# Optimization experiments

Measured on AMD Instinct MI355X. Metric: run time of the kernel, lower is better.

Reference implementation:

```python
import jax, jax.numpy as jnp
import numpy as np

B, N, P, L = 8, 512, 32, 3  # batch, n_node, hidden p, n_layer
NODE_FEAT = 3               # 2 + extra_feat_size(=1)
W_STD = 0.01


def setup_inputs() -> dict:
    key = jax.random.key(0)
    ks = jax.random.split(key, 8)
    x = jax.random.uniform(ks[0], (B, N), dtype=jnp.float32)
    adjacency = jax.random.uniform(ks[1], (B, N, N), dtype=jnp.float32)
    weights = jax.random.normal(ks[2], (B, N, N), dtype=jnp.float32)
    extra_feat = jax.random.normal(ks[3], (B, N, 1), dtype=jnp.float32)
    # per-layer parameters, stacked on a leading layer axis
    t1 = jax.random.normal(ks[4], (L, P, NODE_FEAT), dtype=jnp.float32) * W_STD
    t2 = jax.random.normal(ks[5], (L, P, P), dtype=jnp.float32) * W_STD
    t3 = jax.random.normal(ks[6], (L, P, P), dtype=jnp.float32) * W_STD
    t4 = jax.random.normal(ks[7], (L, P, 4), dtype=jnp.float32) * W_STD
    return {"x": x, "adjacency": adjacency, "weights": weights,
            "extra_feat": extra_feat, "t1": t1, "t2": t2, "t3": t3, "t4": t4}


def reference(x, adjacency, weights, extra_feat, t1, t2, t3, t4):
    b, n = x.shape
    # node features: [1-x, ones, extra_feat]  -> (B, 3, N)
    node_feat = jnp.stack([1.0 - x, jnp.ones_like(x), extra_feat[..., 0]], axis=1)
    # edge features are built from .data in torch => detached
    xd = jax.lax.stop_gradient(x)
    wd = jax.lax.stop_gradient(weights)
    s = 2.0 * xd - 1.0
    is_edge_cut = -(s[:, :, None] * s[:, None, :] - 1.0) * 0.5  # (B,N,N)
    edge_feat = jnp.stack([
        jnp.broadcast_to(xd[:, :, None], (b, n, n)),  # channel 0: x expanded
        wd,                                           # channel 1: weights
        is_edge_cut,                                  # channel 2
        jnp.ones((b, n, n), dtype=x.dtype),           # channel 3: ones
    ], axis=1)  # (B, 4, N, N)

    mu = jnp.zeros((b, t1.shape[1], n), dtype=x.dtype)  # (B, P, N)
    for i in range(t1.shape[0]):
        term1 = jnp.einsum('pf,bfn->bpn', t1[i], node_feat)
        term2 = jnp.einsum('bpn,bnm->bpm',
                           jnp.einsum('pq,bqn->bpn', t2[i], mu), adjacency)
        # skinny 4->P matmul over N*N edges, relu, sum over last axis
        t31 = jax.nn.relu(jnp.einsum('pe,benm->bpnm', t4[i], edge_feat)).sum(-1)  # (B,P,N)
        term3 = jnp.einsum('pq,bqn->bpn', t3[i], t31)
        mu = jax.nn.relu(term1 + term2 + term3)
    return mu
```

## Files before the change

### kernel.cpp

```cpp
#include <hip/hip_runtime.h>

#define BB 8
#define NN 512
#define PP 32
#define SLOT (BB*NN*PP)

__global__ __launch_bounds__(256) void k_phaseA(
    const float* __restrict__ x, const float* __restrict__ wts,
    const float* __restrict__ extra, const float* __restrict__ t1,
    const float* __restrict__ t2, const float* __restrict__ t3,
    const float* __restrict__ t4, float* __restrict__ ws)
{
    const int tid  = threadIdx.x;
    const int wv   = tid >> 6;
    const int lane = tid & 63;
    const int blk  = blockIdx.x;
    const int l  = blk >> 10;
    const int b  = (blk >> 7) & 7;
    const int nt = blk & 127;
    const int n  = nt*4 + wv;

    __shared__ float part[4][32][68];
    __shared__ float cbuf[4][32];

    const float* xrow = x + b*NN;
    const float* wrow = wts + ((size_t)b*NN + n)*NN;
    const float4 wa = *(const float4*)(wrow + lane*4);
    const float4 wb = *(const float4*)(wrow + 256 + lane*4);
    const float4 xa = *(const float4*)(xrow + lane*4);
    const float4 xb = *(const float4*)(xrow + 256 + lane*4);
    const float4 sa = { 2.f*xa.x-1.f, 2.f*xa.y-1.f, 2.f*xa.z-1.f, 2.f*xa.w-1.f };
    const float4 sb = { 2.f*xb.x-1.f, 2.f*xb.y-1.f, 2.f*xb.z-1.f, 2.f*xb.w-1.f };
    const float xn = xrow[n];
    const float en = extra[b*NN + n];
    const float sn = 2.f*xn - 1.f;

    const float* t4l = t4 + l*(PP*4);
#pragma unroll
    for (int p = 0; p < 32; ++p) {
        const float c0 = t4l[p*4+0], Ay = t4l[p*4+1];
        const float Bz = t4l[p*4+2], c3 = t4l[p*4+3];
        const float Cc = fmaf(c0, xn, fmaf(0.5f, Bz, c3));
        const float Bc = -0.5f*Bz*sn;
        float a0, a1;
        a0  = fmaxf(0.f, fmaf(Ay, wa.x, fmaf(Bc, sa.x, Cc)));
        a1  = fmaxf(0.f, fmaf(Ay, wa.y, fmaf(Bc, sa.y, Cc)));
        a0 += fmaxf(0.f, fmaf(Ay, wa.z, fmaf(Bc, sa.z, Cc)));
        a1 += fmaxf(0.f, fmaf(Ay, wa.w, fmaf(Bc, sa.w, Cc)));
        a0 += fmaxf(0.f, fmaf(Ay, wb.x, fmaf(Bc, sb.x, Cc)));
        a1 += fmaxf(0.f, fmaf(Ay, wb.y, fmaf(Bc, sb.y, Cc)));
        a0 += fmaxf(0.f, fmaf(Ay, wb.z, fmaf(Bc, sb.z, Cc)));
        a1 += fmaxf(0.f, fmaf(Ay, wb.w, fmaf(Bc, sb.w, Cc)));
        part[wv][p][lane] = a0 + a1;
    }

    const int p2 = lane & 31, h = lane >> 5;
    float r = 0.f;
#pragma unroll
    for (int k = 0; k < 8; ++k) {
        const float4 v = *(const float4*)&part[wv][p2][h*32 + k*4];
        r += (v.x + v.y) + (v.z + v.w);
    }
    r += __shfl_xor(r, 32, 64);
    cbuf[wv][p2] = r;

    const float* t3r = t3 + l*(PP*PP) + p2*32;
    float term3 = 0.f;
#pragma unroll
    for (int q = 0; q < 8; ++q) {
        const float4 tv = *(const float4*)(t3r + q*4);
        const float4 cv = *(const float4*)&cbuf[wv][q*4];
        term3 = fmaf(tv.x,cv.x, fmaf(tv.y,cv.y, fmaf(tv.z,cv.z, fmaf(tv.w,cv.w, term3))));
    }
    const float* t1r = t1 + l*(PP*3) + p2*3;
    const float term1 = fmaf(t1r[0], 1.f-xn, fmaf(t1r[2], en, t1r[1]));
    const float basev = term1 + term3;

    if (l == 0) {
        const float mu0 = fmaxf(basev, 0.f);
        cbuf[wv][p2] = mu0;
        const float* t2r = t2 + PP*PP + p2*32;
        float s0 = 0.f;
#pragma unroll
        for (int q = 0; q < 8; ++q) {
            const float4 tv = *(const float4*)(t2r + q*4);
            const float4 cv = *(const float4*)&cbuf[wv][q*4];
            s0 = fmaf(tv.x,cv.x, fmaf(tv.y,cv.y, fmaf(tv.z,cv.z, fmaf(tv.w,cv.w, s0))));
        }
        if (h == 0) ws[2*SLOT + ((size_t)(b*NN + n))*PP + p2] = s0;
    } else {
        float* dst = ws + (l == 1 ? 0 : SLOT);
        if (h == 0) dst[((size_t)(b*NN + n))*PP + p2] = basev;
    }
}

__global__ __launch_bounds__(512) void k_layer(
    const float* __restrict__ adj, const float* __restrict__ t2l,
    const float* __restrict__ basein, const float* __restrict__ tmp2in,
    float* __restrict__ tmp2out, float* __restrict__ dout, int final_)
{
    const int tid  = threadIdx.x;
    const int b    = blockIdx.x >> 3;
    const int jt   = blockIdx.x & 7;
    const int j0   = jt * 64;
    const int w    = __builtin_amdgcn_readfirstlane(tid >> 6);
    const int lane = tid & 63;
    const int hh   = w >> 2;
    const int ww   = w & 3;

    __shared__ float part[2][32][66];
    __shared__ float mub[32][66];

    float acc[8];
#pragma unroll
    for (int i = 0; i < 8; ++i) acc[i] = 0.f;

    const float* adjp = adj + (size_t)b*NN*NN + (size_t)(hh*256)*NN + j0 + lane;
    const float* trp  = tmp2in + (size_t)b*NN*PP + (size_t)(hh*256)*PP + ww*8;

#pragma unroll 8
    for (int n = 0; n < 256; ++n) {
        const float av = adjp[(size_t)n*NN];
        const float4 ta = *(const float4*)(trp + n*PP);
        const float4 tb = *(const float4*)(trp + n*PP + 4);
        acc[0] = fmaf(ta.x, av, acc[0]);
        acc[1] = fmaf(ta.y, av, acc[1]);
        acc[2] = fmaf(ta.z, av, acc[2]);
        acc[3] = fmaf(ta.w, av, acc[3]);
        acc[4] = fmaf(tb.x, av, acc[4]);
        acc[5] = fmaf(tb.y, av, acc[5]);
        acc[6] = fmaf(tb.z, av, acc[6]);
        acc[7] = fmaf(tb.w, av, acc[7]);
    }
#pragma unroll
    for (int i = 0; i < 8; ++i) part[hh][ww*8 + i][lane] = acc[i];
    __syncthreads();

    const int j  = tid & 63;
    const int pg = tid >> 6;
    const float4 bs = *(const float4*)(basein + ((size_t)b*NN + j0 + j)*PP + pg*4);
    float r0 = part[0][pg*4+0][j] + part[1][pg*4+0][j] + bs.x;
    float r1 = part[0][pg*4+1][j] + part[1][pg*4+1][j] + bs.y;
    float r2 = part[0][pg*4+2][j] + part[1][pg*4+2][j] + bs.z;
    float r3 = part[0][pg*4+3][j] + part[1][pg*4+3][j] + bs.w;
    r0 = fmaxf(r0, 0.f); r1 = fmaxf(r1, 0.f);
    r2 = fmaxf(r2, 0.f); r3 = fmaxf(r3, 0.f);

    if (final_) {
        dout[((size_t)b*PP + pg*4+0)*NN + j0 + j] = r0;
        dout[((size_t)b*PP + pg*4+1)*NN + j0 + j] = r1;
        dout[((size_t)b*PP + pg*4+2)*NN + j0 + j] = r2;
        dout[((size_t)b*PP + pg*4+3)*NN + j0 + j] = r3;
    } else {
        mub[pg*4+0][j] = r0;
        mub[pg*4+1][j] = r1;
        mub[pg*4+2][j] = r2;
        mub[pg*4+3][j] = r3;
        __syncthreads();

        const float* t0 = t2l + (pg*4+0)*32;
        const float* t1r = t2l + (pg*4+1)*32;
        const float* t2r = t2l + (pg*4+2)*32;
        const float* t3r = t2l + (pg*4+3)*32;
        float o0 = 0.f, o1 = 0.f, o2 = 0.f, o3 = 0.f;
#pragma unroll
        for (int qc = 0; qc < 8; ++qc) {
            const float m0 = mub[qc*4+0][j];
            const float m1 = mub[qc*4+1][j];
            const float m2 = mub[qc*4+2][j];
            const float m3 = mub[qc*4+3][j];
            const float4 a0 = *(const float4*)(t0  + qc*4);
            const float4 a1 = *(const float4*)(t1r + qc*4);
            const float4 a2 = *(const float4*)(t2r + qc*4);
            const float4 a3 = *(const float4*)(t3r + qc*4);
            o0 = fmaf(a0.x,m0, fmaf(a0.y,m1, fmaf(a0.z,m2, fmaf(a0.w,m3, o0))));
            o1 = fmaf(a1.x,m0, fmaf(a1.y,m1, fmaf(a1.z,m2, fmaf(a1.w,m3, o1))));
            o2 = fmaf(a2.x,m0, fmaf(a2.y,m1, fmaf(a2.z,m2, fmaf(a2.w,m3, o2))));
            o3 = fmaf(a3.x,m0, fmaf(a3.y,m1, fmaf(a3.z,m2, fmaf(a3.w,m3, o3))));
        }
        const float4 ov = { o0, o1, o2, o3 };
        *(float4*)(tmp2out + ((size_t)b*NN + j0 + j)*PP + pg*4) = ov;
    }
}

extern "C" void kernel_launch(void* const* d_in, const int* in_sizes, int n_in,
                              void* d_out, int out_size, void* d_ws, size_t ws_size,
                              hipStream_t stream) {
    const float* x     = (const float*)d_in[0];
    const float* adj   = (const float*)d_in[1];
    const float* wts   = (const float*)d_in[2];
    const float* extra = (const float*)d_in[3];
    const float* t1    = (const float*)d_in[4];
    const float* t2    = (const float*)d_in[5];
    const float* t3    = (const float*)d_in[6];
    const float* t4    = (const float*)d_in[7];
    float* out = (float*)d_out;
    float* ws  = (float*)d_ws;

    float* slotA = ws;
    float* slotB = ws + SLOT;
    float* slotC = ws + 2*SLOT;

    hipLaunchKernelGGL(k_phaseA, dim3(3*BB*128), dim3(256), 0, stream,
                       x, wts, extra, t1, t2, t3, t4, ws);
    hipLaunchKernelGGL(k_layer, dim3(BB*8), dim3(512), 0, stream,
                       adj, t2 + 2*PP*PP, slotA, slotC, slotA, (float*)nullptr, 0);
    hipLaunchKernelGGL(k_layer, dim3(BB*8), dim3(512), 0, stream,
                       adj, t2, slotB, slotA, (float*)nullptr, out, 1);
}
```

Before: 146.2 us.

## Split adjacency matmul along N into partial kernels plus reduce; batch phaseA work

Each adjacency layer is split into a partial-product kernel with 256 blocks, each handling a quarter of the N reduction with tmp2 staged in LDS, followed by a small reduce kernel that sums the partials, adds the base, applies relu and computes the next t2 projection. The previous layout used only 64 blocks. Phase A now runs 1024 blocks that each loop over three (layer, batch, node) units and reads t4 from LDS. This raises parallelism on the adjacency pass at the cost of two extra launches and a round trip of the partial sums through global memory.

```diff
diff --git a/kernel.cpp b/kernel.cpp
--- a/kernel.cpp
+++ b/kernel.cpp
@@ -3,7 +3,12 @@
 #define BB 8
 #define NN 512
 #define PP 32
-#define SLOT (BB*NN*PP)
+
+#define OFF_BASE1 0
+#define OFF_BASE2 131072
+#define OFF_T21   262144
+#define OFF_T22   393216
+#define OFF_PART  524288
 
 __global__ __launch_bounds__(256) void k_phaseA(
     const float* __restrict__ x, const float* __restrict__ wts,
@@ -14,115 +19,126 @@
     const int tid  = threadIdx.x;
     const int wv   = tid >> 6;
     const int lane = tid & 63;
-    const int blk  = blockIdx.x;
-    const int l  = blk >> 10;
-    const int b  = (blk >> 7) & 7;
-    const int nt = blk & 127;
-    const int n  = nt*4 + wv;
-
+
+    __shared__ float4 t4lds[3][32];
     __shared__ float part[4][32][68];
     __shared__ float cbuf[4][32];
 
-    const float* xrow = x + b*NN;
-    const float* wrow = wts + ((size_t)b*NN + n)*NN;
-    const float4 wa = *(const float4*)(wrow + lane*4);
-    const float4 wb = *(const float4*)(wrow + 256 + lane*4);
-    const float4 xa = *(const float4*)(xrow + lane*4);
-    const float4 xb = *(const float4*)(xrow + 256 + lane*4);
-    const float4 sa = { 2.f*xa.x-1.f, 2.f*xa.y-1.f, 2.f*xa.z-1.f, 2.f*xa.w-1.f };
-    const float4 sb = { 2.f*xb.x-1.f, 2.f*xb.y-1.f, 2.f*xb.z-1.f, 2.f*xb.w-1.f };
-    const float xn = xrow[n];
-    const float en = extra[b*NN + n];
-    const float sn = 2.f*xn - 1.f;
-
-    const float* t4l = t4 + l*(PP*4);
-#pragma unroll
-    for (int p = 0; p < 32; ++p) {
-        const float c0 = t4l[p*4+0], Ay = t4l[p*4+1];
-        const float Bz = t4l[p*4+2], c3 = t4l[p*4+3];
-        const float Cc = fmaf(c0, xn, fmaf(0.5f, Bz, c3));
-        const float Bc = -0.5f*Bz*sn;
-        float a0, a1;
-        a0  = fmaxf(0.f, fmaf(Ay, wa.x, fmaf(Bc, sa.x, Cc)));
-        a1  = fmaxf(0.f, fmaf(Ay, wa.y, fmaf(Bc, sa.y, Cc)));
-        a0 += fmaxf(0.f, fmaf(Ay, wa.z, fmaf(Bc, sa.z, Cc)));
-        a1 += fmaxf(0.f, fmaf(Ay, wa.w, fmaf(Bc, sa.w, Cc)));
-        a0 += fmaxf(0.f, fmaf(Ay, wb.x, fmaf(Bc, sb.x, Cc)));
-        a1 += fmaxf(0.f, fmaf(Ay, wb.y, fmaf(Bc, sb.y, Cc)));
-        a0 += fmaxf(0.f, fmaf(Ay, wb.z, fmaf(Bc, sb.z, Cc)));
-        a1 += fmaxf(0.f, fmaf(Ay, wb.w, fmaf(Bc, sb.w, Cc)));
-        part[wv][p][lane] = a0 + a1;
-    }
-
-    const int p2 = lane & 31, h = lane >> 5;
-    float r = 0.f;
-#pragma unroll
-    for (int k = 0; k < 8; ++k) {
-        const float4 v = *(const float4*)&part[wv][p2][h*32 + k*4];
-        r += (v.x + v.y) + (v.z + v.w);
-    }
-    r += __shfl_xor(r, 32, 64);
-    cbuf[wv][p2] = r;
-
-    const float* t3r = t3 + l*(PP*PP) + p2*32;
-    float term3 = 0.f;
-#pragma unroll
-    for (int q = 0; q < 8; ++q) {
-        const float4 tv = *(const float4*)(t3r + q*4);
-        const float4 cv = *(const float4*)&cbuf[wv][q*4];
-        term3 = fmaf(tv.x,cv.x, fmaf(tv.y,cv.y, fmaf(tv.z,cv.z, fmaf(tv.w,cv.w, term3))));
-    }
-    const float* t1r = t1 + l*(PP*3) + p2*3;
-    const float term1 = fmaf(t1r[0], 1.f-xn, fmaf(t1r[2], en, t1r[1]));
-    const float basev = term1 + term3;
-
-    if (l == 0) {
-        const float mu0 = fmaxf(basev, 0.f);
-        cbuf[wv][p2] = mu0;
-        const float* t2r = t2 + PP*PP + p2*32;
-        float s0 = 0.f;
+    if (tid < 96) t4lds[0][tid] = ((const float4*)t4)[tid];
+    __syncthreads();
+
+    const int wgid = blockIdx.x * 4 + wv;
+#pragma unroll 1
+    for (int k = 0; k < 3; ++k) {
+        const int u = wgid * 3 + k;
+        const int l = u >> 12;
+        const int b = (u >> 9) & 7;
+        const int n = u & 511;
+
+        const float* xrow = x + b*NN;
+        const float* wrow = wts + ((size_t)b*NN + n)*NN;
+        const float4 wa = *(const float4*)(wrow + lane*4);
+        const float4 wb = *(const float4*)(wrow + 256 + lane*4);
+        const float4 xa = *(const float4*)(xrow + lane*4);
+        const float4 xb = *(const float4*)(xrow + 256 + lane*4);
+        const float4 sa = { 2.f*xa.x-1.f, 2.f*xa.y-1.f, 2.f*xa.z-1.f, 2.f*xa.w-1.f };
+        const float4 sb = { 2.f*xb.x-1.f, 2.f*xb.y-1.f, 2.f*xb.z-1.f, 2.f*xb.w-1.f };
+        const float xn = xrow[n];
+        const float en = extra[b*NN + n];
+        const float sn = 2.f*xn - 1.f;
+
+#pragma unroll
+        for (int p = 0; p < 32; ++p) {
+            const float4 c4 = t4lds[l][p];
+            const float Ay = c4.y;
+            const float Cc = fmaf(c4.x, xn, fmaf(0.5f, c4.z, c4.w));
+            const float Bc = -0.5f*c4.z*sn;
+            float a0, a1;
+            a0  = fmaxf(0.f, fmaf(Ay, wa.x, fmaf(Bc, sa.x, Cc)));
+            a1  = fmaxf(0.f, fmaf(Ay, wa.y, fmaf(Bc, sa.y, Cc)));
+            a0 += fmaxf(0.f, fmaf(Ay, wa.z, fmaf(Bc, sa.z, Cc)));
+            a1 += fmaxf(0.f, fmaf(Ay, wa.w, fmaf(Bc, sa.w, Cc)));
+            a0 += fmaxf(0.f, fmaf(Ay, wb.x, fmaf(Bc, sb.x, Cc)));
+            a1 += fmaxf(0.f, fmaf(Ay, wb.y, fmaf(Bc, sb.y, Cc)));
+            a0 += fmaxf(0.f, fmaf(Ay, wb.z, fmaf(Bc, sb.z, Cc)));
+            a1 += fmaxf(0.f, fmaf(Ay, wb.w, fmaf(Bc, sb.w, Cc)));
+            part[wv][p][lane] = a0 + a1;
+        }
+
+        const int p2 = lane & 31, h = lane >> 5;
+        float r = 0.f;
 #pragma unroll
         for (int q = 0; q < 8; ++q) {
-            const float4 tv = *(const float4*)(t2r + q*4);
+            const float4 v = *(const float4*)&part[wv][p2][h*32 + q*4];
+            r += (v.x + v.y) + (v.z + v.w);
+        }
+        r += __shfl_xor(r, 32, 64);
+        cbuf[wv][p2] = r;
+
+        const float* t3r = t3 + l*(PP*PP) + p2*32;
+        float term3 = 0.f;
+#pragma unroll
+        for (int q = 0; q < 8; ++q) {
+            const float4 tv = *(const float4*)(t3r + q*4);
             const float4 cv = *(const float4*)&cbuf[wv][q*4];
-            s0 = fmaf(tv.x,cv.x, fmaf(tv.y,cv.y, fmaf(tv.z,cv.z, fmaf(tv.w,cv.w, s0))));
-        }
-        if (h == 0) ws[2*SLOT + ((size_t)(b*NN + n))*PP + p2] = s0;
-    } else {
-        float* dst = ws + (l == 1 ? 0 : SLOT);
-        if (h == 0) dst[((size_t)(b*NN + n))*PP + p2] = basev;
-    }
-}
-
-__global__ __launch_bounds__(512) void k_layer(
-    const float* __restrict__ adj, const float* __restrict__ t2l,
-    const float* __restrict__ basein, const float* __restrict__ tmp2in,
-    float* __restrict__ tmp2out, float* __restrict__ dout, int final_)
+            term3 = fmaf(tv.x,cv.x, fmaf(tv.y,cv.y, fmaf(tv.z,cv.z, fmaf(tv.w,cv.w, term3))));
+        }
+        const float* t1r = t1 + l*(PP*3) + p2*3;
+        const float term1 = fmaf(t1r[0], 1.f-xn, fmaf(t1r[2], en, t1r[1]));
+        const float basev = term1 + term3;
+
+        if (l == 0) {
+            const float mu0 = fmaxf(basev, 0.f);
+            cbuf[wv][p2] = mu0;
+            const float* t2r = t2 + PP*PP + p2*32;
+            float s0 = 0.f;
+#pragma unroll
+            for (int q = 0; q < 8; ++q) {
+                const float4 tv = *(const float4*)(t2r + q*4);
+                const float4 cv = *(const float4*)&cbuf[wv][q*4];
+                s0 = fmaf(tv.x,cv.x, fmaf(tv.y,cv.y, fmaf(tv.z,cv.z, fmaf(tv.w,cv.w, s0))));
+            }
+            if (h == 0) ws[OFF_T21 + ((size_t)(b*NN + n))*PP + p2] = s0;
+        } else {
+            float* dst = ws + (l == 1 ? OFF_BASE1 : OFF_BASE2);
+            if (h == 0) dst[((size_t)(b*NN + n))*PP + p2] = basev;
+        }
+    }
+}
+
+__global__ __launch_bounds__(512) void k_partial(
+    const float* __restrict__ adj, const float* __restrict__ tmp2in,
+    float* __restrict__ partout, int b_, int unused)
 {
-    const int tid  = threadIdx.x;
-    const int b    = blockIdx.x >> 3;
-    const int jt   = blockIdx.x & 7;
-    const int j0   = jt * 64;
-    const int w    = __builtin_amdgcn_readfirstlane(tid >> 6);
-    const int lane = tid & 63;
-    const int hh   = w >> 2;
-    const int ww   = w & 3;
-
-    __shared__ float part[2][32][66];
-    __shared__ float mub[32][66];
-
-    float acc[8];
-#pragma unroll
-    for (int i = 0; i < 8; ++i) acc[i] = 0.f;
-
-    const float* adjp = adj + (size_t)b*NN*NN + (size_t)(hh*256)*NN + j0 + lane;
-    const float* trp  = tmp2in + (size_t)b*NN*PP + (size_t)(hh*256)*PP + ww*8;
-
+    const int tid = threadIdx.x;
+    const int blk = blockIdx.x;
+    const int b   = blk >> 5;
+    const int jt  = (blk >> 2) & 7;
+    const int nq  = blk & 3;
+    const int w   = tid >> 6;
+    const int lane= tid & 63;
+    const int ww  = w & 3;
+    const int hh  = w >> 2;
+
+    __shared__ float tlds[128*32];
+    __shared__ float comb[2][32][66];
+
+    const float* src = tmp2in + ((size_t)b*NN + nq*128)*PP;
+#pragma unroll
+    for (int t = 0; t < 2; ++t) {
+        const int i4 = t*512 + tid;
+        ((float4*)tlds)[i4] = ((const float4*)src)[i4];
+    }
+    __syncthreads();
+
+    float acc[8] = {0.f,0.f,0.f,0.f,0.f,0.f,0.f,0.f};
+    const float* adjp = adj + ((size_t)b*NN + nq*128 + hh*64)*NN + jt*64 + lane;
+    const float* trow = tlds + (hh*64)*32 + ww*8;
 #pragma unroll 8
-    for (int n = 0; n < 256; ++n) {
-        const float av = adjp[(size_t)n*NN];
-        const float4 ta = *(const float4*)(trp + n*PP);
-        const float4 tb = *(const float4*)(trp + n*PP + 4);
+    for (int i = 0; i < 64; ++i) {
+        const float av = adjp[(size_t)i*NN];
+        const float4 ta = *(const float4*)(trow + i*32);
+        const float4 tb = *(const float4*)(trow + i*32 + 4);
         acc[0] = fmaf(ta.x, av, acc[0]);
         acc[1] = fmaf(ta.y, av, acc[1]);
         acc[2] = fmaf(ta.z, av, acc[2]);
@@ -133,53 +149,78 @@
         acc[7] = fmaf(tb.w, av, acc[7]);
     }
 #pragma unroll
-    for (int i = 0; i < 8; ++i) part[hh][ww*8 + i][lane] = acc[i];
+    for (int t = 0; t < 8; ++t) comb[hh][ww*8 + t][lane] = acc[t];
     __syncthreads();
 
     const int j  = tid & 63;
     const int pg = tid >> 6;
-    const float4 bs = *(const float4*)(basein + ((size_t)b*NN + j0 + j)*PP + pg*4);
-    float r0 = part[0][pg*4+0][j] + part[1][pg*4+0][j] + bs.x;
-    float r1 = part[0][pg*4+1][j] + part[1][pg*4+1][j] + bs.y;
-    float r2 = part[0][pg*4+2][j] + part[1][pg*4+2][j] + bs.z;
-    float r3 = part[0][pg*4+3][j] + part[1][pg*4+3][j] + bs.w;
-    r0 = fmaxf(r0, 0.f); r1 = fmaxf(r1, 0.f);
-    r2 = fmaxf(r2, 0.f); r3 = fmaxf(r3, 0.f);
+    float4 o;
+    o.x = comb[0][pg*4+0][j] + comb[1][pg*4+0][j];
+    o.y = comb[0][pg*4+1][j] + comb[1][pg*4+1][j];
+    o.z = comb[0][pg*4+2][j] + comb[1][pg*4+2][j];
+    o.w = comb[0][pg*4+3][j] + comb[1][pg*4+3][j];
+    float* pdst = partout + ((((size_t)nq*BB + b)*8 + jt)*64 + j)*PP + pg*4;
+    *(float4*)pdst = o;
+}
+
+__global__ __launch_bounds__(512) void k_reduce(
+    const float* __restrict__ basein, const float* __restrict__ partin,
+    const float* __restrict__ t2l, float* __restrict__ tmp2out,
+    float* __restrict__ dout, int final_)
+{
+    const int tid = threadIdx.x;
+    const int b   = blockIdx.x >> 3;
+    const int jt  = blockIdx.x & 7;
+    const int j   = tid & 63;
+    const int pg  = tid >> 6;
+
+    __shared__ float muT[32][66];
+
+    const size_t pbase = ((((size_t)b)*8 + jt)*64 + j)*PP + pg*4;
+    const float4 s0 = *(const float4*)(partin + pbase);
+    const float4 s1 = *(const float4*)(partin + 131072 + pbase);
+    const float4 s2 = *(const float4*)(partin + 262144 + pbase);
+    const float4 s3 = *(const float4*)(partin + 393216 + pbase);
+    const float4 bs = *(const float4*)(basein + ((size_t)b*NN + jt*64 + j)*PP + pg*4);
+    float r0 = fmaxf((s0.x+s1.x) + (s2.x+s3.x) + bs.x, 0.f);
+    float r1 = fmaxf((s0.y+s1.y) + (s2.y+s3.y) + bs.y, 0.f);
+    float r2 = fmaxf((s0.z+s1.z) + (s2.z+s3.z) + bs.z, 0.f);
+    float r3 = fmaxf((s0.w+s1.w) + (s2.w+s3.w) + bs.w, 0.f);
 
     if (final_) {
-        dout[((size_t)b*PP + pg*4+0)*NN + j0 + j] = r0;
-        dout[((size_t)b*PP + pg*4+1)*NN + j0 + j] = r1;
-        dout[((size_t)b*PP + pg*4+2)*NN + j0 + j] = r2;
-        dout[((size_t)b*PP + pg*4+3)*NN + j0 + j] = r3;
+        dout[((size_t)b*PP + pg*4+0)*NN + jt*64 + j] = r0;
+        dout[((size_t)b*PP + pg*4+1)*NN + jt*64 + j] = r1;
+        dout[((size_t)b*PP + pg*4+2)*NN + jt*64 + j] = r2;
+        dout[((size_t)b*PP + pg*4+3)*NN + jt*64 + j] = r3;
     } else {
-        mub[pg*4+0][j] = r0;
-        mub[pg*4+1][j] = r1;
-        mub[pg*4+2][j] = r2;
-        mub[pg*4+3][j] = r3;
+        muT[pg*4+0][j] = r0;
+        muT[pg*4+1][j] = r1;
+        muT[pg*4+2][j] = r2;
+        muT[pg*4+3][j] = r3;
         __syncthreads();
 
-        const float* t0 = t2l + (pg*4+0)*32;
-        const float* t1r = t2l + (pg*4+1)*32;
-        const float* t2r = t2l + (pg*4+2)*32;
-        const float* t3r = t2l + (pg*4+3)*32;
-        float o0 = 0.f, o1 = 0.f, o2 = 0.f, o3 = 0.f;
+        const float* ta = t2l + (pg*4+0)*32;
+        const float* tb = t2l + (pg*4+1)*32;
+        const float* tc = t2l + (pg*4+2)*32;
+        const float* td = t2l + (pg*4+3)*32;
+        float o0=0.f, o1=0.f, o2=0.f, o3=0.f;
 #pragma unroll
         for (int qc = 0; qc < 8; ++qc) {
-            const float m0 = mub[qc*4+0][j];
-            const float m1 = mub[qc*4+1][j];
-            const float m2 = mub[qc*4+2][j];
-            const float m3 = mub[qc*4+3][j];
-            const float4 a0 = *(const float4*)(t0  + qc*4);
-            const float4 a1 = *(const float4*)(t1r + qc*4);
-            const float4 a2 = *(const float4*)(t2r + qc*4);
-            const float4 a3 = *(const float4*)(t3r + qc*4);
+            const float m0 = muT[qc*4+0][j];
+            const float m1 = muT[qc*4+1][j];
+            const float m2 = muT[qc*4+2][j];
+            const float m3 = muT[qc*4+3][j];
+            const float4 a0 = *(const float4*)(ta + qc*4);
+            const float4 a1 = *(const float4*)(tb + qc*4);
+            const float4 a2 = *(const float4*)(tc + qc*4);
+            const float4 a3 = *(const float4*)(td + qc*4);
             o0 = fmaf(a0.x,m0, fmaf(a0.y,m1, fmaf(a0.z,m2, fmaf(a0.w,m3, o0))));
             o1 = fmaf(a1.x,m0, fmaf(a1.y,m1, fmaf(a1.z,m2, fmaf(a1.w,m3, o1))));
             o2 = fmaf(a2.x,m0, fmaf(a2.y,m1, fmaf(a2.z,m2, fmaf(a2.w,m3, o2))));
             o3 = fmaf(a3.x,m0, fmaf(a3.y,m1, fmaf(a3.z,m2, fmaf(a3.w,m3, o3))));
         }
         const float4 ov = { o0, o1, o2, o3 };
-        *(float4*)(tmp2out + ((size_t)b*NN + j0 + j)*PP + pg*4) = ov;
+        *(float4*)(tmp2out + ((size_t)b*NN + jt*64 + j)*PP + pg*4) = ov;
     }
 }
 
@@ -197,14 +238,20 @@
     float* out = (float*)d_out;
     float* ws  = (float*)d_ws;
 
-    float* slotA = ws;
-    float* slotB = ws + SLOT;
-    float* slotC = ws + 2*SLOT;
-
-    hipLaunchKernelGGL(k_phaseA, dim3(3*BB*128), dim3(256), 0, stream,
+    float* base1 = ws + OFF_BASE1;
+    float* base2 = ws + OFF_BASE2;
+    float* t21   = ws + OFF_T21;
+    float* t22   = ws + OFF_T22;
+    float* part  = ws + OFF_PART;
+
+    hipLaunchKernelGGL(k_phaseA, dim3(1024), dim3(256), 0, stream,
                        x, wts, extra, t1, t2, t3, t4, ws);
-    hipLaunchKernelGGL(k_layer, dim3(BB*8), dim3(512), 0, stream,
-                       adj, t2 + 2*PP*PP, slotA, slotC, slotA, (float*)nullptr, 0);
-    hipLaunchKernelGGL(k_layer, dim3(BB*8), dim3(512), 0, stream,
-                       adj, t2, slotB, slotA, (float*)nullptr, out, 1);
-}
+    hipLaunchKernelGGL(k_partial, dim3(256), dim3(512), 0, stream,
+                       adj, t21, part, 0, 0);
+    hipLaunchKernelGGL(k_reduce, dim3(64), dim3(512), 0, stream,
+                       base1, part, t2 + 2*PP*PP, t22, (float*)nullptr, 0);
+    hipLaunchKernelGGL(k_partial, dim3(256), dim3(512), 0, stream,
+                       adj, t22, part, 0, 0);
+    hipLaunchKernelGGL(k_reduce, dim3(64), dim3(512), 0, stream,
+                       base2, part, (const float*)t2, (float*)nullptr, out, 1);
+}
```

Result: faster. 121.6 us (-16.8%).
